# Kernel optimization log

Measured on AMD Instinct MI355X. Metric: run time of the kernel, lower is better.

The kernel has to match this reference:

```python
import jax, jax.numpy as jnp
import numpy as np

LN_EPS = 1e-12


def _layernorm(x, gamma, beta):
    mu = jnp.mean(x, axis=-1, keepdims=True)
    var = jnp.mean((x - mu) ** 2, axis=-1, keepdims=True)
    return (x - mu) * jax.lax.rsqrt(var + LN_EPS) * gamma + beta


def _gcn(x, node_emb, time_emb, wpool, bpool, ln_g, ln_b):
    # x: [B,N,C]; node_emb: [N,D]; time_emb: [D]
    e = _layernorm(node_emb + time_emb[None, :], ln_g, ln_b)          # [N,D] (dropout in eval = identity)
    adj = jax.nn.softmax(e @ e.T, axis=1)                             # [N,N] dynamic adjacency
    weights = jnp.einsum('nd,dkio->nkio', e, wpool)                   # [N,2,Cin,Cout] per-node weights
    bias = e @ bpool                                                  # [N,Cout]
    # supports = [I, adj]: identity support is just x itself
    x_g = jnp.stack([x, jnp.einsum('nm,bmc->bnc', adj, x)], axis=2)   # [B,N,2,Cin]
    return jnp.einsum('bnki,nkio->bno', x_g, weights) + bias          # [B,N,Cout]


def setup_inputs() -> dict:
    key = jax.random.key(0)
    ks = jax.random.split(key, 10)
    B, N, Cin, H, D = 32, 2048, 32, 64, 64
    s = 0.1
    return {
        'x': jax.random.normal(ks[0], (B, N, Cin), jnp.float32),
        'state': jax.random.normal(ks[1], (B, N, H), jnp.float32),
        'node_embeddings': jax.random.normal(ks[2], (N, D), jnp.float32),
        'time_embeddings': jax.random.normal(ks[3], (D,), jnp.float32),
        'gate_wpool': jax.random.normal(ks[4], (D, 2, Cin + H, 2 * H), jnp.float32) * s,
        'gate_bpool': jax.random.normal(ks[5], (D, 2 * H), jnp.float32) * s,
        'gate_ln_g': jnp.ones((D,), jnp.float32),
        'gate_ln_b': jnp.zeros((D,), jnp.float32),
        'update_wpool': jax.random.normal(ks[6], (D, 2, Cin + H, H), jnp.float32) * s,
        'update_bpool': jax.random.normal(ks[7], (D, H), jnp.float32) * s,
        'update_ln_g': jnp.ones((D,), jnp.float32),
        'update_ln_b': jnp.zeros((D,), jnp.float32),
    }


def reference(x, state, node_embeddings, time_embeddings,
              gate_wpool, gate_bpool, gate_ln_g, gate_ln_b,
              update_wpool, update_bpool, update_ln_g, update_ln_b):
    H = state.shape[-1]
    inp = jnp.concatenate([x, state], axis=-1)                        # [B,N,Cin+H]
    z_r = jax.nn.sigmoid(_gcn(inp, node_embeddings, time_embeddings,
                              gate_wpool, gate_bpool, gate_ln_g, gate_ln_b))
    z, r = z_r[..., :H], z_r[..., H:]
    cand = jnp.concatenate([x, z * state], axis=-1)
    hc = jnp.tanh(_gcn(cand, node_embeddings, time_embeddings,
                       update_wpool, update_bpool, update_ln_g, update_ln_b))
    return r * state + (1.0 - r) * hc
```

## Files before the change

### kernel.cpp

```cpp
#include <hip/hip_runtime.h>

typedef _Float16 f16;
typedef _Float16 half8 __attribute__((ext_vector_type(8)));
typedef float f32x4 __attribute__((ext_vector_type(4)));

#define NN 2048
#define BB 32
#define CINC 32
#define HH 64
#define DD 64
#define C1 96
#define KI 192
#define OG 128
#define OU 64
#define WCG 24576
#define WCU 12288

#define XGI(n, ks, b, kk) (((((size_t)(n)) * 6 + (ks)) * BB + (b)) * 32 + (kk))
#define STHI(n, b, o) ((((size_t)(n)) * BB + (b)) * HH + (o))

__device__ __forceinline__ f32x4 mfma16(half8 a, half8 b, f32x4 c) {
  return __builtin_amdgcn_mfma_f32_16x16x32_f16(a, b, c, 0, 0, 0);
}

typedef __attribute__((address_space(1))) const void* gas_t;
typedef __attribute__((address_space(3))) void* las_t;
__device__ __forceinline__ void gl_lds16(const void* g, void* l) {
  __builtin_amdgcn_global_load_lds((gas_t)g, (las_t)l, 16, 0, 0);
}

#define SWZ(row, kb) (((row) << 7) + ((kb) ^ (((row) & 7) << 4)))

__global__ __launch_bounds__(256) void k_prep(
    const float* __restrict__ ne, const float* __restrict__ te,
    const float* __restrict__ gg, const float* __restrict__ gb,
    const float* __restrict__ ug, const float* __restrict__ ub,
    const float* __restrict__ gbp, const float* __restrict__ ubp,
    const float* __restrict__ gwp, const float* __restrict__ uwp,
    const float* __restrict__ x, const float* __restrict__ st,
    f16* __restrict__ egh, f16* __restrict__ euh,
    float* __restrict__ biasg, float* __restrict__ biasu,
    f16* __restrict__ wtg, f16* __restrict__ wtu,
    f16* __restrict__ cm, f16* __restrict__ xg, f16* __restrict__ sth) {
  __shared__ __align__(16) char smem[12672];
  const int bid = blockIdx.x;
  const int t = threadIdx.x;
  if (bid < 512) {
    float (*esg)[64] = (float(*)[64])smem;
    float (*esu)[64] = (float(*)[64])(smem + 1024);
    int nl = t >> 6;
    int node = bid * 4 + nl;
    int d = t & 63;
    float v = ne[node * DD + d] + te[d];
    float s = v;
    #pragma unroll
    for (int m = 1; m < 64; m <<= 1) s += __shfl_xor(s, m, 64);
    float mu = s * (1.f / 64.f);
    float df = v - mu;
    float q = df * df;
    #pragma unroll
    for (int m = 1; m < 64; m <<= 1) q += __shfl_xor(q, m, 64);
    float rs = rsqrtf(q * (1.f / 64.f) + 1e-12f);
    float base = df * rs;
    float a = base * gg[d] + gb[d];
    float b = base * ug[d] + ub[d];
    egh[node * DD + d] = (f16)a;
    euh[node * DD + d] = (f16)b;
    esg[nl][d] = a; esu[nl][d] = b;
    __syncthreads();
    #pragma unroll
    for (int i = 0; i < 3; ++i) {
      int u = i * 256 + t;
      int un = u / 192, oo = u % 192;
      int n2 = bid * 4 + un;
      float acc = 0.f;
      if (oo < OG) {
        #pragma unroll 8
        for (int dd = 0; dd < 64; ++dd) acc += esg[un][dd] * gbp[dd * OG + oo];
        biasg[(size_t)n2 * OG + oo] = acc;
      } else {
        int o = oo - OG;
        #pragma unroll 8
        for (int dd = 0; dd < 64; ++dd) acc += esu[un][dd] * ubp[dd * OU + o];
        biasu[(size_t)n2 * OU + o] = acc;
      }
    }
  } else if (bid < 512 + 2304) {
    float (*tile)[17] = (float(*)[17])smem;
    const int t2 = bid - 512;
    const int ki = t2 % 192;
    const int oy = t2 / 192;
    const int upd = oy >= 8;
    const float* wpool = upd ? uwp : gwp;
    f16* wt = upd ? wtu : wtg;
    const int O = upd ? OU : OG;
    const int o0 = (upd ? oy - 8 : oy) * 16;
    const int ks = ki >> 5, kk = ki & 31;
    #pragma unroll
    for (int i = 0; i < 4; ++i) {
      int e2 = i * 256 + t;
      int d = e2 >> 4, o = e2 & 15;
      tile[d][o] = wpool[((size_t)d * KI + ki) * O + o0 + o];
    }
    __syncthreads();
    #pragma unroll
    for (int i = 0; i < 4; ++i) {
      int e2 = i * 256 + t;
      int o = e2 >> 6, d = e2 & 63;
      size_t row = ((size_t)ks * O + (o0 + o)) * 32 + kk;
      wt[row * DD + d] = (f16)tile[d][o];
    }
  } else {
    f16 (*tile)[66] = (f16(*)[66])smem;
    const int t2 = bid - 2816;
    const int mb = (t2 & 31) * 64;
    const int b = t2 >> 5;
    #pragma unroll
    for (int i = 0; i < 24; ++i) {
      int e2 = i * 256 + t;
      int m = e2 / 96, c = e2 % 96;
      float v = (c < CINC) ? x[((size_t)b * NN + mb + m) * CINC + c]
                           : st[((size_t)b * NN + mb + m) * HH + c - CINC];
      f16 h = (f16)v;
      tile[c][m] = h;
      xg[XGI(mb + m, c >> 5, b, c & 31)] = h;
      if (c >= CINC) sth[STHI(mb + m, b, c - CINC)] = h;
    }
    __syncthreads();
    #pragma unroll
    for (int i = 0; i < 24; ++i) {
      int e2 = i * 256 + t;
      int c = e2 >> 6, m = e2 & 63;
      cm[((size_t)b * C1 + c) * NN + mb + m] = tile[c][m];
    }
  }
}

__global__ __launch_bounds__(256) void k_transpose_zs(const f16* __restrict__ zs,
                                                      f16* __restrict__ cm) {
  __shared__ f16 tile[64][66];
  int mb = blockIdx.x * 64;
  int b = blockIdx.y;
  int t = threadIdx.x;
  #pragma unroll
  for (int i = 0; i < 16; ++i) {
    int e2 = i * 256 + t;
    int m = e2 >> 6, o = e2 & 63;
    tile[o][m] = zs[((size_t)b * NN + mb + m) * HH + o];
  }
  __syncthreads();
  #pragma unroll
  for (int i = 0; i < 16; ++i) {
    int e2 = i * 256 + t;
    int o = e2 >> 6, m = e2 & 63;
    cm[((size_t)b * C1 + CINC + o) * NN + mb + m] = tile[o][m];
  }
}

__global__ __launch_bounds__(256) void k_attn(const f16* __restrict__ eg,
                                              const f16* __restrict__ eu,
                                              f16* __restrict__ adjg,
                                              f16* __restrict__ adju) {
  const f16* eh = blockIdx.y ? eu : eg;
  f16* adj = blockIdx.y ? adju : adjg;
  const int r0 = blockIdx.x * 16;
  const int w = threadIdx.x >> 6, lane = threadIdx.x & 63;
  const int fr = lane & 15, fq = lane >> 4;
  __shared__ float pm[4][16], ps[4][16];
  __shared__ float fm[16], fs[16];
  const half8 a0 = *(const half8*)&eh[(size_t)(r0 + fr) * DD + fq * 8];
  const half8 a1 = *(const half8*)&eh[(size_t)(r0 + fr) * DD + 32 + fq * 8];
  float m[4], s[4];
  #pragma unroll
  for (int r = 0; r < 4; ++r) { m[r] = -3.0e38f; s[r] = 0.f; }
  for (int ct = 0; ct < 32; ++ct) {
    const int c0 = w * 512 + ct * 16;
    half8 b0 = *(const half8*)&eh[(size_t)(c0 + fr) * DD + fq * 8];
    half8 b1 = *(const half8*)&eh[(size_t)(c0 + fr) * DD + 32 + fq * 8];
    f32x4 d = mfma16(a0, b0, f32x4{0.f, 0.f, 0.f, 0.f});
    d = mfma16(a1, b1, d);
    #pragma unroll
    for (int r = 0; r < 4; ++r) {
      float mn = fmaxf(m[r], d[r]);
      s[r] = s[r] * __expf(m[r] - mn) + __expf(d[r] - mn);
      m[r] = mn;
    }
  }
  #pragma unroll
  for (int r = 0; r < 4; ++r) {
    #pragma unroll
    for (int mk = 1; mk < 16; mk <<= 1) {
      float mo = __shfl_xor(m[r], mk, 64);
      float so = __shfl_xor(s[r], mk, 64);
      float mn = fmaxf(m[r], mo);
      s[r] = s[r] * __expf(m[r] - mn) + so * __expf(mo - mn);
      m[r] = mn;
    }
  }
  if (fr == 0) {
    #pragma unroll
    for (int r = 0; r < 4; ++r) { pm[w][fq * 4 + r] = m[r]; ps[w][fq * 4 + r] = s[r]; }
  }
  __syncthreads();
  if (threadIdx.x < 16) {
    float M = -3.0e38f;
    #pragma unroll
    for (int i = 0; i < 4; ++i) M = fmaxf(M, pm[i][threadIdx.x]);
    float S = 0.f;
    #pragma unroll
    for (int i = 0; i < 4; ++i) S += ps[i][threadIdx.x] * __expf(pm[i][threadIdx.x] - M);
    fm[threadIdx.x] = M; fs[threadIdx.x] = 1.f / S;
  }
  __syncthreads();
  float Mr[4], Sr[4];
  #pragma unroll
  for (int r = 0; r < 4; ++r) { Mr[r] = fm[fq * 4 + r]; Sr[r] = fs[fq * 4 + r]; }
  for (int ct = 0; ct < 32; ++ct) {
    const int c0 = w * 512 + ct * 16;
    half8 b0 = *(const half8*)&eh[(size_t)(c0 + fr) * DD + fq * 8];
    half8 b1 = *(const half8*)&eh[(size_t)(c0 + fr) * DD + 32 + fq * 8];
    f32x4 d = mfma16(a0, b0, f32x4{0.f, 0.f, 0.f, 0.f});
    d = mfma16(a1, b1, d);
    #pragma unroll
    for (int r = 0; r < 4; ++r)
      adj[(size_t)(r0 + fq * 4 + r) * NN + c0 + fr] = (f16)(__expf(d[r] - Mr[r]) * Sr[r]);
  }
}

#define BM 64
#define BN 96

__global__ __launch_bounds__(256, 4) void k_gemm_xa(const f16* __restrict__ A,
                                                    const f16* __restrict__ Bm,
                                                    f16* __restrict__ xg) {
  const int orig = blockIdx.x;
  const int xcd = orig & 7, j = orig >> 3;
  const int nb = (j >> 2) * BM;
  const int by = (xcd << 2) + (j & 3);
  const int cb = by * BN;
  const int tid = threadIdx.x;
  const int w = tid >> 6, lane = tid & 63;
  const int wr = (w >> 1) * 32, wc = (w & 1) * 48;
  const int fr = lane & 15, fq = lane >> 4;

  const int arow = tid >> 3;
  const int acolb = ((tid & 7) * 16) ^ ((arow & 7) << 4);
  const char* asrc = (const char*)A + (size_t)(nb + arow) * (NN * 2) + acolb;
  const char* bsrc = (const char*)Bm + (size_t)(cb + arow) * (NN * 2) + acolb;

  __shared__ f16 Al[2][BM * 64];
  __shared__ f16 Bl[2][BN * 64];
  auto stage = [&](int buf, int kt) {
    const size_t ko = (size_t)kt * 2;
    char* ad = (char*)&Al[buf][0] + (w << 10);
    char* bd = (char*)&Bl[buf][0] + (w << 10);
    gl_lds16(asrc + ko, ad);
    gl_lds16(asrc + ko + (size_t)32 * (NN * 2), ad + 4096);
    gl_lds16(bsrc + ko, bd);
    gl_lds16(bsrc + ko + (size_t)32 * (NN * 2), bd + 4096);
    gl_lds16(bsrc + ko + (size_t)64 * (NN * 2), bd + 8192);
  };

  f32x4 acc[2][3] = {};
  stage(0, 0);
  for (int kt = 0; kt < NN; kt += 64) {
    const int cur = (kt >> 6) & 1;
    if (kt + 64 < NN) {
      stage(cur ^ 1, kt + 64);
      asm volatile("s_waitcnt vmcnt(5)" ::: "memory");
    } else {
      asm volatile("s_waitcnt vmcnt(0)" ::: "memory");
    }
    __builtin_amdgcn_sched_barrier(0);
    __builtin_amdgcn_s_barrier();
    const char* Ab = (const char*)&Al[cur][0];
    const char* Bb = (const char*)&Bl[cur][0];
    half8 af[2][2], bf[2][3];
    #pragma unroll
    for (int k0 = 0; k0 < 2; ++k0) {
      const int kb = k0 * 64 + fq * 16;
      #pragma unroll
      for (int mt = 0; mt < 2; ++mt)
        af[k0][mt] = *(const half8*)(Ab + SWZ(wr + mt * 16 + fr, kb));
      #pragma unroll
      for (int nt = 0; nt < 3; ++nt)
        bf[k0][nt] = *(const half8*)(Bb + SWZ(wc + nt * 16 + fr, kb));
    }
    asm volatile("s_waitcnt lgkmcnt(0)" ::: "memory");
    __builtin_amdgcn_sched_barrier(0);
    __builtin_amdgcn_s_barrier();
    #pragma unroll
    for (int k0 = 0; k0 < 2; ++k0)
      #pragma unroll
      for (int mt = 0; mt < 2; ++mt)
        #pragma unroll
        for (int nt = 0; nt < 3; ++nt)
          acc[mt][nt] = mfma16(af[k0][mt], bf[k0][nt], acc[mt][nt]);
  }
  #pragma unroll
  for (int mt = 0; mt < 2; ++mt)
    #pragma unroll
    for (int nt = 0; nt < 3; ++nt)
      #pragma unroll
      for (int r = 0; r < 4; ++r) {
        int n = nb + wr + mt * 16 + fq * 4 + r;
        int l = wc + nt * 16 + fr;
        xg[XGI(n, 3 + (l >> 5), by, l & 31)] = (f16)acc[mt][nt][r];
      }
}

__global__ __launch_bounds__(256) void k_gemm_w2(const f16* __restrict__ A,
                                                 const f16* __restrict__ B,
                                                 f16* __restrict__ W, int ncols) {
  __shared__ f16 Al[128 * 64];
  __shared__ f16 Bl[128 * 64];
  const int cb = blockIdx.x * 128;
  const int nb = blockIdx.y * 128;
  const int tid = threadIdx.x;
  const int w = tid >> 6, lane = tid & 63;
  const int wr = (w >> 1) * 64, wc = (w & 1) * 64;
  const int fr = lane & 15, fq = lane >> 4;
  const int arow = tid >> 3;
  const int acolb = ((tid & 7) * 16) ^ ((arow & 7) << 4);
  const char* asrc = (const char*)A + (size_t)(nb + arow) * 128 + acolb;
  const char* bsrc = (const char*)B + (size_t)(cb + arow) * 128 + acolb;
  char* ad = (char*)Al + (w << 10);
  char* bd = (char*)Bl + (w << 10);
  #pragma unroll
  for (int j = 0; j < 4; ++j) gl_lds16(asrc + (size_t)j * 32 * 128, ad + j * 4096);
  #pragma unroll
  for (int j = 0; j < 4; ++j) gl_lds16(bsrc + (size_t)j * 32 * 128, bd + j * 4096);
  __syncthreads();
  f32x4 acc[4][4] = {};
  #pragma unroll
  for (int k0 = 0; k0 < 2; ++k0) {
    const int kb = k0 * 64 + fq * 16;
    half8 af[4], bf[4];
    #pragma unroll
    for (int mt = 0; mt < 4; ++mt)
      af[mt] = *(const half8*)((const char*)Al + SWZ(wr + mt * 16 + fr, kb));
    #pragma unroll
    for (int nt = 0; nt < 4; ++nt)
      bf[nt] = *(const half8*)((const char*)Bl + SWZ(wc + nt * 16 + fr, kb));
    #pragma unroll
    for (int mt = 0; mt < 4; ++mt)
      #pragma unroll
      for (int nt = 0; nt < 4; ++nt)
        acc[mt][nt] = mfma16(af[mt], bf[nt], acc[mt][nt]);
  }
  #pragma unroll
  for (int mt = 0; mt < 4; ++mt)
    #pragma unroll
    for (int nt = 0; nt < 4; ++nt)
      #pragma unroll
      for (int r = 0; r < 4; ++r) {
        int n = nb + wr + mt * 16 + fq * 4 + r;
        int c = cb + wc + nt * 16 + fr;
        W[(size_t)n * ncols + c] = (f16)acc[mt][nt][r];
      }
}

template <bool GATE>
__global__ __launch_bounds__(256) void k_apply3(
    const f16* __restrict__ xg, const f16* __restrict__ W,
    const float* __restrict__ bias,
    const f16* __restrict__ sth,
    f16* xgw, f16* __restrict__ zs, f16* __restrict__ rbuf,
    float* __restrict__ outp) {
  constexpr int O = GATE ? OG : OU;
  constexpr int WS = GATE ? WCG : WCU;
  constexpr int NOT_ = GATE ? 2 : 1;
  const int n = blockIdx.x;
  const int lane = threadIdx.x & 63, w = threadIdx.x >> 6;
  const int fr = lane & 15, fq = lane >> 4;
  half8 af[2][6];
  #pragma unroll
  for (int mt = 0; mt < 2; ++mt) {
    #pragma unroll
    for (int ks = 0; ks < 6; ++ks)
      af[mt][ks] = *(const half8*)&xg[XGI(n, ks, mt * 16 + fr, fq * 8)];
  }
  if (GATE) __syncthreads();
  f32x4 acc[2][NOT_] = {};
  #pragma unroll
  for (int ks = 0; ks < 6; ++ks) {
    #pragma unroll
    for (int ot = 0; ot < NOT_; ++ot) {
      int o = (GATE ? (w * 2 + ot) : w) * 16 + fr;
      half8 bf = *(const half8*)&W[(size_t)n * WS + (((size_t)ks * O + o) << 5) + fq * 8];
      #pragma unroll
      for (int mt = 0; mt < 2; ++mt) acc[mt][ot] = mfma16(af[mt][ks], bf, acc[mt][ot]);
    }
  }
  #pragma unroll
  for (int mt = 0; mt < 2; ++mt)
    #pragma unroll
    for (int ot = 0; ot < NOT_; ++ot) {
      const int o = (GATE ? (w * 2 + ot) : w) * 16 + fr;
      const float bs = bias[(size_t)n * O + o];
      #pragma unroll
      for (int r = 0; r < 4; ++r) {
        int b = mt * 16 + fq * 4 + r;
        float val = acc[mt][ot][r] + bs;
        if (GATE) {
          float s = 1.f / (1.f + expf(-val));
          if (o < HH) {
            float zst = s * (float)sth[STHI(n, b, o)];
            xgw[XGI(n, 1 + (o >> 5), b, o & 31)] = (f16)zst;
            zs[((size_t)b * NN + n) * HH + o] = (f16)zst;
          } else {
            rbuf[STHI(n, b, o - HH)] = (f16)s;
          }
        } else {
          float hc = tanhf(val);
          float rr = (float)rbuf[STHI(n, b, o)];
          outp[((size_t)b * NN + n) * HH + o] =
              rr * (float)sth[STHI(n, b, o)] + (1.f - rr) * hc;
        }
      }
    }
}

extern "C" void kernel_launch(void* const* d_in, const int* in_sizes, int n_in,
                              void* d_out, int out_size, void* d_ws, size_t ws_size,
                              hipStream_t stream) {
  const float* x   = (const float*)d_in[0];
  const float* st  = (const float*)d_in[1];
  const float* ne  = (const float*)d_in[2];
  const float* te  = (const float*)d_in[3];
  const float* gwp = (const float*)d_in[4];
  const float* gbp = (const float*)d_in[5];
  const float* gg  = (const float*)d_in[6];
  const float* gb  = (const float*)d_in[7];
  const float* uwp = (const float*)d_in[8];
  const float* ubp = (const float*)d_in[9];
  const float* ug  = (const float*)d_in[10];
  const float* ub  = (const float*)d_in[11];
  float* out = (float*)d_out;

  char* wsb = (char*)d_ws;
  size_t off = 0;
  auto alloc = [&](size_t bytes) {
    char* p = wsb + off;
    off = (off + bytes + 255) & ~(size_t)255;
    return p;
  };
  f16*   egh   = (f16*)  alloc((size_t)NN * DD * 2);
  f16*   euh   = (f16*)  alloc((size_t)NN * DD * 2);
  float* biasg = (float*)alloc((size_t)NN * OG * 4);
  float* biasu = (float*)alloc((size_t)NN * OU * 4);
  f16*   wtg   = (f16*)  alloc((size_t)WCG * DD * 2);
  f16*   wtu   = (f16*)  alloc((size_t)WCU * DD * 2);
  f16*   xg    = (f16*)  alloc((size_t)NN * BB * KI * 2);
  f16*   cm    = (f16*)  alloc((size_t)BB * C1 * NN * 2);
  f16*   zs    = (f16*)  alloc((size_t)BB * NN * HH * 2);
  f16*   rbuf  = (f16*)  alloc((size_t)BB * NN * HH * 2);
  f16*   sth   = (f16*)  alloc((size_t)BB * NN * HH * 2);
  f16*   adj   = (f16*)  alloc((size_t)NN * NN * 2);
  f16*   adju  = (f16*)  alloc((size_t)NN * NN * 2);
  f16*   W     = (f16*)  alloc((size_t)NN * WCG * 2);
  (void)ws_size; (void)in_sizes; (void)n_in; (void)out_size;

  hipLaunchKernelGGL(k_prep, dim3(512 + 2304 + 1024), dim3(256), 0, stream,
                     ne, te, gg, gb, ug, ub, gbp, ubp, gwp, uwp, x, st,
                     egh, euh, biasg, biasu, wtg, wtu, cm, xg, sth);
  hipLaunchKernelGGL(k_attn, dim3(NN / 16, 2), dim3(256), 0, stream,
                     egh, euh, adj, adju);

  hipLaunchKernelGGL(k_gemm_xa, dim3(1024), dim3(256), 0, stream, adj, cm, xg);
  hipLaunchKernelGGL(k_gemm_w2, dim3(WCG / 128, NN / 128), dim3(256), 0, stream,
                     egh, wtg, W, WCG);
  hipLaunchKernelGGL((k_apply3<true>), dim3(NN), dim3(256), 0, stream,
                     xg, W, biasg, sth, xg, zs, rbuf, (float*)nullptr);
  hipLaunchKernelGGL(k_transpose_zs, dim3(NN / 64, BB), dim3(256), 0, stream, zs, cm);

  hipLaunchKernelGGL(k_gemm_xa, dim3(1024), dim3(256), 0, stream, adju, cm, xg);
  hipLaunchKernelGGL(k_gemm_w2, dim3(WCU / 128, NN / 128), dim3(256), 0, stream,
                     euh, wtu, W, WCU);
  hipLaunchKernelGGL((k_apply3<false>), dim3(NN), dim3(256), 0, stream,
                     xg, W, biasu, sth, (f16*)nullptr, (f16*)nullptr, rbuf, out);
}
```

Baseline: 194.8 us.

## Fuse adjacency-x GEMM with both per-node weight GEMMs into one interleaved launch

Merges the first adj@x GEMM and the gate and update per-node weight GEMMs into one kernel. Blocks are interleaved 1:4 so the compute-heavy xa tiles and the store-heavy weight-generation tiles run on the CUs at the same time. The update weights are now computed early into a separate buffer, which removes one launch and lets the later update phase skip its weight GEMM. The cost is extra workspace for a second weight buffer, and the w2 blocks now run with 40KB of static LDS and the xa launch bounds.

```diff
diff --git a/kernel.cpp b/kernel.cpp
--- a/kernel.cpp
+++ b/kernel.cpp
@@ -230,10 +230,9 @@
 #define BM 64
 #define BN 96
 
-__global__ __launch_bounds__(256, 4) void k_gemm_xa(const f16* __restrict__ A,
-                                                    const f16* __restrict__ Bm,
-                                                    f16* __restrict__ xg) {
-  const int orig = blockIdx.x;
+__device__ __forceinline__ void xa_body(int orig, const f16* __restrict__ A,
+                                        const f16* __restrict__ Bm,
+                                        f16* __restrict__ xg, char* smem) {
   const int xcd = orig & 7, j = orig >> 3;
   const int nb = (j >> 2) * BM;
   const int by = (xcd << 2) + (j & 3);
@@ -248,8 +247,8 @@
   const char* asrc = (const char*)A + (size_t)(nb + arow) * (NN * 2) + acolb;
   const char* bsrc = (const char*)Bm + (size_t)(cb + arow) * (NN * 2) + acolb;
 
-  __shared__ f16 Al[2][BM * 64];
-  __shared__ f16 Bl[2][BN * 64];
+  f16 (*Al)[BM * 64] = (f16(*)[BM * 64])smem;
+  f16 (*Bl)[BN * 64] = (f16(*)[BN * 64])(smem + 16384);
   auto stage = [&](int buf, int kt) {
     const size_t ko = (size_t)kt * 2;
     char* ad = (char*)&Al[buf][0] + (w << 10);
@@ -309,13 +308,11 @@
       }
 }
 
-__global__ __launch_bounds__(256) void k_gemm_w2(const f16* __restrict__ A,
-                                                 const f16* __restrict__ B,
-                                                 f16* __restrict__ W, int ncols) {
-  __shared__ f16 Al[128 * 64];
-  __shared__ f16 Bl[128 * 64];
-  const int cb = blockIdx.x * 128;
-  const int nb = blockIdx.y * 128;
+__device__ __forceinline__ void w2_body(int cb, int nb, const f16* __restrict__ A,
+                                        const f16* __restrict__ B,
+                                        f16* __restrict__ W, int ncols, char* smem) {
+  f16* Al = (f16*)smem;
+  f16* Bl = (f16*)(smem + 16384);
   const int tid = threadIdx.x;
   const int w = tid >> 6, lane = tid & 63;
   const int wr = (w >> 1) * 64, wc = (w & 1) * 64;
@@ -358,6 +355,37 @@
         int c = cb + wc + nt * 16 + fr;
         W[(size_t)n * ncols + c] = (f16)acc[mt][nt][r];
       }
+}
+
+__global__ __launch_bounds__(256, 4) void k_mega1(
+    const f16* __restrict__ adjg, const f16* __restrict__ cm, f16* __restrict__ xg,
+    const f16* __restrict__ egh, const f16* __restrict__ wtg, f16* __restrict__ Wg,
+    const f16* __restrict__ euh, const f16* __restrict__ wtu, f16* __restrict__ Wu) {
+  __shared__ __align__(16) char smem[40960];
+  const int bid = blockIdx.x;
+  int xa_id = -1, w2_id = -1;
+  if (bid < 5120) {
+    int q = bid / 5, r = bid % 5;
+    if (r == 0) xa_id = q;
+    else w2_id = q * 4 + (r - 1);
+  } else {
+    w2_id = 4096 + (bid - 5120);
+  }
+  if (xa_id >= 0) {
+    xa_body(xa_id, adjg, cm, xg, smem);
+  } else if (w2_id < 3072) {
+    w2_body((w2_id % 192) * 128, (w2_id / 192) * 128, egh, wtg, Wg, WCG, smem);
+  } else {
+    int u = w2_id - 3072;
+    w2_body((u % 96) * 128, (u / 96) * 128, euh, wtu, Wu, WCU, smem);
+  }
+}
+
+__global__ __launch_bounds__(256, 4) void k_gemm_xa(const f16* __restrict__ A,
+                                                    const f16* __restrict__ Bm,
+                                                    f16* __restrict__ xg) {
+  __shared__ __align__(16) char smem[40960];
+  xa_body(blockIdx.x, A, Bm, xg, smem);
 }
 
 template <bool GATE>
@@ -458,7 +486,8 @@
   f16*   sth   = (f16*)  alloc((size_t)BB * NN * HH * 2);
   f16*   adj   = (f16*)  alloc((size_t)NN * NN * 2);
   f16*   adju  = (f16*)  alloc((size_t)NN * NN * 2);
-  f16*   W     = (f16*)  alloc((size_t)NN * WCG * 2);
+  f16*   Wg    = (f16*)  alloc((size_t)NN * WCG * 2);
+  f16*   Wu    = (f16*)  alloc((size_t)NN * WCU * 2);
   (void)ws_size; (void)in_sizes; (void)n_in; (void)out_size;
 
   hipLaunchKernelGGL(k_prep, dim3(512 + 2304 + 1024), dim3(256), 0, stream,
@@ -467,16 +496,13 @@
   hipLaunchKernelGGL(k_attn, dim3(NN / 16, 2), dim3(256), 0, stream,
                      egh, euh, adj, adju);
 
-  hipLaunchKernelGGL(k_gemm_xa, dim3(1024), dim3(256), 0, stream, adj, cm, xg);
-  hipLaunchKernelGGL(k_gemm_w2, dim3(WCG / 128, NN / 128), dim3(256), 0, stream,
-                     egh, wtg, W, WCG);
+  hipLaunchKernelGGL(k_mega1, dim3(5632), dim3(256), 0, stream,
+                     adj, cm, xg, egh, wtg, Wg, euh, wtu, Wu);
   hipLaunchKernelGGL((k_apply3<true>), dim3(NN), dim3(256), 0, stream,
-                     xg, W, biasg, sth, xg, zs, rbuf, (float*)nullptr);
+                     xg, Wg, biasg, sth, xg, zs, rbuf, (float*)nullptr);
   hipLaunchKernelGGL(k_transpose_zs, dim3(NN / 64, BB), dim3(256), 0, stream, zs, cm);
 
   hipLaunchKernelGGL(k_gemm_xa, dim3(1024), dim3(256), 0, stream, adju, cm, xg);
-  hipLaunchKernelGGL(k_gemm_w2, dim3(WCU / 128, NN / 128), dim3(256), 0, stream,
-                     euh, wtu, W, WCU);
   hipLaunchKernelGGL((k_apply3<false>), dim3(NN), dim3(256), 0, stream,
-                     xg, W, biasu, sth, (f16*)nullptr, (f16*)nullptr, rbuf, out);
-}
+                     xg, Wu, biasu, sth, (f16*)nullptr, (f16*)nullptr, rbuf, out);
+}
```

Result: slower. 204.6 us (+5.1%).
